# Kernel optimization log

Hardware: AMD Instinct MI355X
Metric: run time of the kernel (lower is better)

Reference implementation:

```python
import jax, jax.numpy as jnp
import numpy as np

NUM_USERS = 100000
NUM_ITEMS = 50000
EMBED_DIM = 64
N_LAYERS = 3
NNZ = 4800000
BATCH = 16384
N_NODES = NUM_USERS + NUM_ITEMS


def setup_inputs() -> dict:
    key = jax.random.key(0)
    k1, k2, k3, k4, k5, k6, k7 = jax.random.split(key, 7)
    users = jax.random.randint(k1, (BATCH,), 0, NUM_USERS, dtype=jnp.int64 if jax.config.jax_enable_x64 else jnp.int32)
    items = jax.random.randint(k2, (BATCH,), 0, NUM_ITEMS, dtype=jnp.int64 if jax.config.jax_enable_x64 else jnp.int32)
    adj_rows = jax.random.randint(k3, (NNZ,), 0, N_NODES, dtype=jnp.int32)
    adj_cols = jax.random.randint(k4, (NNZ,), 0, N_NODES, dtype=jnp.int32)
    adj_vals = jax.random.uniform(k5, (NNZ,), dtype=jnp.float32)
    user_emb = jax.random.normal(k6, (NUM_USERS, EMBED_DIM), dtype=jnp.float32)
    item_emb = jax.random.normal(k7, (NUM_ITEMS, EMBED_DIM), dtype=jnp.float32)
    return {"users": users, "items": items, "adj_rows": adj_rows,
            "adj_cols": adj_cols, "adj_vals": adj_vals,
            "user_emb": user_emb, "item_emb": item_emb}


def _spmm(rows, cols, vals, x):
    # y = A @ x for COO sparse A: gather source rows, scale, scatter-add to dest
    return jax.ops.segment_sum(vals[:, None] * x[cols], rows, num_segments=N_NODES)


def reference(users, items, adj_rows, adj_cols, adj_vals, user_emb, item_emb):
    ego = jnp.concatenate([user_emb, item_emb], axis=0)  # [N_NODES, D]
    acc = ego
    cur = ego
    for _ in range(N_LAYERS):
        cur = _spmm(adj_rows, adj_cols, adj_vals, cur)
        acc = acc + cur
    mean_emb = acc / jnp.float32(N_LAYERS + 1)
    user_final = mean_emb[:NUM_USERS]
    item_final = mean_emb[NUM_USERS:]
    u = user_final[users]  # [B, D]
    i = item_final[items]  # [B, D]
    return jnp.sum(u * i, axis=-1)  # [B]
```

## Files before the change

kernel.cpp:

```cpp
#include <hip/hip_runtime.h>
#include <hip/hip_bf16.h>

#define NUM_USERS 100000
#define NUM_ITEMS 50000
#define EMBED_DIM 64
#define N_NODES   150000
#define ROW_SHIFT 10
#define ROWS_PER_BUCKET 1024
#define B_BUCKETS ((N_NODES + ROWS_PER_BUCKET - 1) / ROWS_PER_BUCKET)
#define BIN_CHUNK 2048
#define COL_MASK 0x3FFFF
#define NSTRIPE 5
#define STRIPE_SHIFT 15

typedef unsigned short ushort_t;
typedef unsigned int uint_t;

__device__ __forceinline__ float bf16_to_f32(ushort_t u) {
    return __uint_as_float(((unsigned)u) << 16);
}
__device__ __forceinline__ ushort_t f32_to_bf16(float f) {
    return __builtin_bit_cast(ushort_t, __float2bfloat16(f));
}
__device__ __forceinline__ float bflo(uint_t r) {
    return __uint_as_float(r << 16);
}
__device__ __forceinline__ float bfhi(uint_t r) {
    return __uint_as_float(r & 0xffff0000u);
}

__global__ void k_bucket_hist(const int* __restrict__ rows, int* __restrict__ bhist, int nnz) {
    __shared__ int lh[256];
    int t = threadIdx.x;
    lh[t] = 0;
    __syncthreads();
    int base = blockIdx.x * (256 * 32);
#pragma unroll
    for (int k = 0; k < 32; k++) {
        int idx = base + k * 256 + t;
        if (idx < nnz) atomicAdd(&lh[rows[idx] >> ROW_SHIFT], 1);
    }
    __syncthreads();
    if (t < B_BUCKETS && lh[t] > 0) atomicAdd(&bhist[t], lh[t]);
}

__global__ void k_bucket_scan(const int* __restrict__ bhist, int* __restrict__ bucket_off,
                              int* __restrict__ bucket_cursor, int* __restrict__ offs, int nnz) {
    __shared__ int lds[256];
    int t = threadIdx.x;
    int v = (t < B_BUCKETS) ? bhist[t] : 0;
    lds[t] = v;
    __syncthreads();
    for (int d = 1; d < 256; d <<= 1) {
        int y = (t >= d) ? lds[t - d] : 0;
        __syncthreads();
        lds[t] += y;
        __syncthreads();
    }
    int excl = lds[t] - v;
    if (t < B_BUCKETS) {
        bucket_off[t] = excl;
        bucket_cursor[t] = excl;
    }
    if (t == 0) {
        bucket_off[B_BUCKETS] = nnz;
        offs[N_NODES] = nnz;
    }
}

__global__ void __launch_bounds__(256) k_bin(const int* __restrict__ rows,
                                             const int* __restrict__ cols,
                                             const float* __restrict__ vals,
                                             int* __restrict__ bucket_cursor,
                                             int2* __restrict__ staging, int nnz) {
    __shared__ int  ccnt[256];
    __shared__ int  cpos[256];
    __shared__ int  gdst[256];
    __shared__ int2 entries[BIN_CHUNK];
    __shared__ unsigned char ebuck[BIN_CHUNK];

    int t = threadIdx.x;
    int base = blockIdx.x * BIN_CHUNK;
    ccnt[t] = 0;
    __syncthreads();

    int myrow[BIN_CHUNK / 256];
#pragma unroll
    for (int k = 0; k < BIN_CHUNK / 256; k++) {
        int idx = base + k * 256 + t;
        int r = (idx < nnz) ? rows[idx] : -1;
        myrow[k] = r;
        if (r >= 0) atomicAdd(&ccnt[r >> ROW_SHIFT], 1);
    }
    __syncthreads();

    int c = ccnt[t];
    cpos[t] = c;
    __syncthreads();
    for (int d = 1; d < 256; d <<= 1) {
        int y = (t >= d) ? cpos[t - d] : 0;
        __syncthreads();
        cpos[t] += y;
        __syncthreads();
    }
    int total = cpos[255];
    int excl = cpos[t] - c;
    __syncthreads();
    cpos[t] = excl;
    __syncthreads();

#pragma unroll
    for (int k = 0; k < BIN_CHUNK / 256; k++) {
        int r = myrow[k];
        if (r >= 0) {
            int idx = base + k * 256 + t;
            int b = r >> ROW_SHIFT;
            int lrow = r & (ROWS_PER_BUCKET - 1);
            int slot = atomicAdd(&cpos[b], 1);
            entries[slot] = make_int2(cols[idx] | (lrow << 18), __float_as_int(vals[idx]));
            ebuck[slot] = (unsigned char)b;
        }
    }
    __syncthreads();

    if (t < B_BUCKETS && ccnt[t] > 0) {
        int g = atomicAdd(&bucket_cursor[t], ccnt[t]);
        gdst[t] = g - (cpos[t] - ccnt[t]);
    }
    __syncthreads();

    for (int i = t; i < total; i += 256) {
        staging[gdst[ebuck[i]] + i] = entries[i];
    }
}

__global__ void __launch_bounds__(1024) k_scatter2(const int2* __restrict__ staging,
                                                   const int* __restrict__ bucket_off,
                                                   int* __restrict__ offs,
                                                   int2* __restrict__ cv) {
    __shared__ int rc[ROWS_PER_BUCKET * NSTRIPE];
    __shared__ int sh[ROWS_PER_BUCKET];
    int b = blockIdx.x;
    int t = threadIdx.x;
    int beg = bucket_off[b], end = bucket_off[b + 1];
    int row0 = b << ROW_SHIFT;

#pragma unroll
    for (int s = 0; s < NSTRIPE; s++) rc[t * NSTRIPE + s] = 0;
    __syncthreads();
    for (int i = beg + t; i < end; i += 1024) {
        int ex = staging[i].x;
        int lrow = ex >> 18;
        int stripe = (ex & COL_MASK) >> STRIPE_SHIFT;
        atomicAdd(&rc[lrow * NSTRIPE + stripe], 1);
    }
    __syncthreads();

    int tot = 0;
#pragma unroll
    for (int s = 0; s < NSTRIPE; s++) tot += rc[t * NSTRIPE + s];
    sh[t] = tot;
    __syncthreads();
    for (int d = 1; d < 1024; d <<= 1) {
        int y = (t >= d) ? sh[t - d] : 0;
        __syncthreads();
        sh[t] += y;
        __syncthreads();
    }
    int excl_row = sh[t] - tot;
    int row = row0 + t;
    if (row < N_NODES) offs[row] = beg + excl_row;
    int basec = excl_row;
#pragma unroll
    for (int s = 0; s < NSTRIPE; s++) {
        int cnt = rc[t * NSTRIPE + s];
        rc[t * NSTRIPE + s] = basec;
        basec += cnt;
    }
    __syncthreads();

    for (int i = beg + t; i < end; i += 1024) {
        int2 e = staging[i];
        int lrow = e.x >> 18;
        int col = e.x & COL_MASK;
        int stripe = col >> STRIPE_SHIFT;
        int pos = beg + atomicAdd(&rc[lrow * NSTRIPE + stripe], 1);
        cv[pos] = make_int2(col, e.y);
    }
}

__global__ void k_convert(const float* __restrict__ ue, const float* __restrict__ ie,
                          ushort_t* __restrict__ xb) {
    int i = blockIdx.x * blockDim.x + threadIdx.x;
    const int n4 = (N_NODES * EMBED_DIM) / 4;
    if (i >= n4) return;
    const int usplit = (NUM_USERS * EMBED_DIM) / 4;
    float4 f = (i < usplit) ? ((const float4*)ue)[i] : ((const float4*)ie)[i - usplit];
    ushort4 o;
    o.x = f32_to_bf16(f.x);
    o.y = f32_to_bf16(f.y);
    o.z = f32_to_bf16(f.z);
    o.w = f32_to_bf16(f.w);
    ((ushort4*)xb)[i] = o;
}

__device__ __forceinline__ float2 spmm_row(int beg, int end, int hl, bool hi_half,
                                           const int2* __restrict__ cv,
                                           const ushort_t* __restrict__ xb) {
    const uint_t* __restrict__ xw = (const uint_t*)xb;
    float ax = 0.f, ay = 0.f;
    int e = beg;
    int npair = (end - beg) >> 1;
    int ng = npair >> 3;

    if (ng > 0) {
        uint_t r0[8], r1[8];
        float ve0[8], vo0[8], ve1[8], vo1[8];
#pragma unroll
        for (int j = 0; j < 8; j++) {
            int2 c0 = cv[e + 2 * j];
            int2 c1 = cv[e + 2 * j + 1];
            int ce = __builtin_amdgcn_readfirstlane(c0.x);
            int co = __builtin_amdgcn_readfirstlane(c1.x);
            ve0[j] = __int_as_float(__builtin_amdgcn_readfirstlane(c0.y));
            vo0[j] = __int_as_float(__builtin_amdgcn_readfirstlane(c1.y));
            int col = hi_half ? co : ce;
            r0[j] = xw[(size_t)col * 32 + hl];
        }
        e += 16;
#pragma unroll 1
        for (int g = 1; g < ng; g++) {
#pragma unroll
            for (int j = 0; j < 8; j++) {
                int2 c0 = cv[e + 2 * j];
                int2 c1 = cv[e + 2 * j + 1];
                int ce = __builtin_amdgcn_readfirstlane(c0.x);
                int co = __builtin_amdgcn_readfirstlane(c1.x);
                ve1[j] = __int_as_float(__builtin_amdgcn_readfirstlane(c0.y));
                vo1[j] = __int_as_float(__builtin_amdgcn_readfirstlane(c1.y));
                int col = hi_half ? co : ce;
                r1[j] = xw[(size_t)col * 32 + hl];
            }
            e += 16;
#pragma unroll
            for (int j = 0; j < 8; j++) {
                float v = hi_half ? vo0[j] : ve0[j];
                ax += v * bflo(r0[j]);
                ay += v * bfhi(r0[j]);
            }
#pragma unroll
            for (int j = 0; j < 8; j++) {
                r0[j] = r1[j]; ve0[j] = ve1[j]; vo0[j] = vo1[j];
            }
        }
#pragma unroll
        for (int j = 0; j < 8; j++) {
            float v = hi_half ? vo0[j] : ve0[j];
            ax += v * bflo(r0[j]);
            ay += v * bfhi(r0[j]);
        }
    }
#pragma unroll 1
    for (; e + 2 <= end; e += 2) {
        int2 c0 = cv[e];
        int2 c1 = cv[e + 1];
        int ce = __builtin_amdgcn_readfirstlane(c0.x);
        int co = __builtin_amdgcn_readfirstlane(c1.x);
        float ve = __int_as_float(__builtin_amdgcn_readfirstlane(c0.y));
        float vo = __int_as_float(__builtin_amdgcn_readfirstlane(c1.y));
        int col = hi_half ? co : ce;
        uint_t r = xw[(size_t)col * 32 + hl];
        float v = hi_half ? vo : ve;
        ax += v * bflo(r);
        ay += v * bfhi(r);
    }
    if (e < end) {
        int2 c = cv[e];
        int ce = __builtin_amdgcn_readfirstlane(c.x);
        float ve = __int_as_float(__builtin_amdgcn_readfirstlane(c.y));
        uint_t r = xw[(size_t)ce * 32 + hl];
        float v = hi_half ? 0.f : ve;
        ax += v * bflo(r);
        ay += v * bfhi(r);
    }
    ax += __shfl_xor(ax, 32, 64);
    ay += __shfl_xor(ay, 32, 64);
    return make_float2(ax, ay);
}

__global__ void k_spmm(const int* __restrict__ offs, const int2* __restrict__ cv,
                       const ushort_t* __restrict__ xb, ushort_t* __restrict__ out) {
    int row = (blockIdx.x * blockDim.x + threadIdx.x) >> 6;
    int lane = threadIdx.x & 63;
    if (row >= N_NODES) return;
    int hl = lane & 31;
    bool hi_half = lane >= 32;
    row = __builtin_amdgcn_readfirstlane(row);
    int beg = __builtin_amdgcn_readfirstlane(offs[row]);
    int end = __builtin_amdgcn_readfirstlane(offs[row + 1]);
    float2 a = spmm_row(beg, end, hl, hi_half, cv, xb);
    if (!hi_half) {
        uint_t packed = ((uint_t)f32_to_bf16(a.y) << 16) | (uint_t)f32_to_bf16(a.x);
        ((uint_t*)out)[(size_t)row * 32 + hl] = packed;
    }
}

__global__ void k_spmm_batch(const int* __restrict__ offs, const int2* __restrict__ cv,
                             const ushort_t* __restrict__ xb,
                             const int* __restrict__ users, const int* __restrict__ items,
                             float* __restrict__ u_acc, float* __restrict__ i_acc,
                             int batch) {
    int w = (blockIdx.x * blockDim.x + threadIdx.x) >> 6;
    int lane = threadIdx.x & 63;
    if (w >= 2 * batch) return;
    int hl = lane & 31;
    bool hi_half = lane >= 32;
    int b, row;
    float* dst;
    if (w < batch) { b = w;         row = users[b];             dst = u_acc; }
    else           { b = w - batch; row = NUM_USERS + items[b]; dst = i_acc; }
    row = __builtin_amdgcn_readfirstlane(row);
    int beg = __builtin_amdgcn_readfirstlane(offs[row]);
    int end = __builtin_amdgcn_readfirstlane(offs[row + 1]);
    float2 a = spmm_row(beg, end, hl, hi_half, cv, xb);
    if (!hi_half) {
        float2* d = (float2*)(dst + (size_t)b * EMBED_DIM) + hl;
        float2 cur = *d;
        cur.x += a.x;
        cur.y += a.y;
        *d = cur;
    }
}

__global__ void k_gather_f32(const int* __restrict__ users, const int* __restrict__ items,
                             const float* __restrict__ ue, const float* __restrict__ ie,
                             float* __restrict__ u_acc, float* __restrict__ i_acc, int batch) {
    int w = (blockIdx.x * blockDim.x + threadIdx.x) >> 6;
    int lane = threadIdx.x & 63;
    if (w >= batch) return;
    int nu = users[w];
    int ni = items[w];
    size_t o = (size_t)w * EMBED_DIM + lane;
    u_acc[o] = ue[(size_t)nu * EMBED_DIM + lane];
    i_acc[o] = ie[(size_t)ni * EMBED_DIM + lane];
}

__global__ void k_gather_bf16(const int* __restrict__ users, const int* __restrict__ items,
                              const ushort_t* __restrict__ xb,
                              float* __restrict__ u_acc, float* __restrict__ i_acc, int batch) {
    int w = (blockIdx.x * blockDim.x + threadIdx.x) >> 6;
    int lane = threadIdx.x & 63;
    if (w >= batch) return;
    int nu = users[w];
    int ni = NUM_USERS + items[w];
    size_t o = (size_t)w * EMBED_DIM + lane;
    u_acc[o] += bf16_to_f32(xb[(size_t)nu * EMBED_DIM + lane]);
    i_acc[o] += bf16_to_f32(xb[(size_t)ni * EMBED_DIM + lane]);
}

__global__ void k_dot(const float* __restrict__ u_acc, const float* __restrict__ i_acc,
                      float* __restrict__ out, int batch) {
    int w = (blockIdx.x * blockDim.x + threadIdx.x) >> 6;
    int lane = threadIdx.x & 63;
    if (w >= batch) return;
    size_t o = (size_t)w * EMBED_DIM + lane;
    float p = u_acc[o] * i_acc[o];
#pragma unroll
    for (int d = 32; d > 0; d >>= 1) p += __shfl_down(p, d, 64);
    if (lane == 0) out[w] = p * (1.0f / 16.0f);
}


extern "C" void kernel_launch(void* const* d_in, const int* in_sizes, int n_in,
                              void* d_out, int out_size, void* d_ws, size_t ws_size,
                              hipStream_t stream) {
    const int*   users    = (const int*)  d_in[0];
    const int*   items    = (const int*)  d_in[1];
    const int*   adj_rows = (const int*)  d_in[2];
    const int*   adj_cols = (const int*)  d_in[3];
    const float* adj_vals = (const float*)d_in[4];
    const float* user_emb = (const float*)d_in[5];
    const float* item_emb = (const float*)d_in[6];
    float* out = (float*)d_out;

    const int batch = in_sizes[0];
    const int nnz   = in_sizes[2];

    char* p = (char*)d_ws;
    auto alloc = [&](size_t bytes) -> char* {
        char* r = p;
        p += (bytes + 255) & ~(size_t)255;
        return r;
    };
    const size_t xb_bytes = (size_t)N_NODES * EMBED_DIM * 2;
    int*      offs          = (int*)  alloc(((size_t)N_NODES + 1) * 4);
    int*      bhist         = (int*)  alloc(256 * 4);
    int*      bucket_off    = (int*)  alloc(256 * 4);
    int*      bucket_cursor = (int*)  alloc(256 * 4);
    int2*     cv            = (int2*) alloc((size_t)nnz * 8);
    size_t    region_bytes  = (size_t)nnz * 8;
    if (region_bytes < 2 * xb_bytes) region_bytes = 2 * xb_bytes;
    char*     region        = alloc(region_bytes);
    int2*     staging       = (int2*)region;
    ushort_t* xbA           = (ushort_t*)region;
    ushort_t* xbB           = (ushort_t*)(region + xb_bytes);
    ushort_t* xb_ego        = (ushort_t*)alloc(xb_bytes);
    float*    u_acc         = (float*)alloc((size_t)batch * EMBED_DIM * 4);
    float*    i_acc         = (float*)alloc((size_t)batch * EMBED_DIM * 4);

    const int g_bhist  = (nnz + 256 * 32 - 1) / (256 * 32);
    const int g_bin    = (nnz + BIN_CHUNK - 1) / BIN_CHUNK;
    const int g_conv   = ((N_NODES * EMBED_DIM / 4) + 255) / 256;
    const int g_nodes  = (N_NODES + 3) / 4;
    const int g_batch  = (batch + 3) / 4;
    const int g_batch2 = (2 * batch + 3) / 4;

    hipMemsetAsync(bhist, 0, 256 * 4, stream);
    k_bucket_hist<<<g_bhist, 256, 0, stream>>>(adj_rows, bhist, nnz);
    k_bucket_scan<<<1, 256, 0, stream>>>(bhist, bucket_off, bucket_cursor, offs, nnz);
    k_bin<<<g_bin, 256, 0, stream>>>(adj_rows, adj_cols, adj_vals, bucket_cursor, staging, nnz);
    k_scatter2<<<B_BUCKETS, 1024, 0, stream>>>(staging, bucket_off, offs, cv);

    k_convert<<<g_conv, 256, 0, stream>>>(user_emb, item_emb, xb_ego);

    k_gather_f32<<<g_batch, 256, 0, stream>>>(users, items, user_emb, item_emb,
                                              u_acc, i_acc, batch);

    k_spmm<<<g_nodes, 256, 0, stream>>>(offs, cv, xb_ego, xbA);
    k_gather_bf16<<<g_batch, 256, 0, stream>>>(users, items, xbA, u_acc, i_acc, batch);

    k_spmm<<<g_nodes, 256, 0, stream>>>(offs, cv, xbA, xbB);
    k_gather_bf16<<<g_batch, 256, 0, stream>>>(users, items, xbB, u_acc, i_acc, batch);

    k_spmm_batch<<<g_batch2, 256, 0, stream>>>(offs, cv, xbB, users, items,
                                               u_acc, i_acc, batch);

    k_dot<<<g_batch, 256, 0, stream>>>(u_acc, i_acc, out, batch);
}
```

Baseline: 512.8 us.

## Halve bucket size, drop column striping in CSR build, double-buffer SpMM loads

The COO-to-CSR bucketing now uses 512-row buckets (293 buckets) with 512-thread blocks, and removes the per-row column-stripe sub-sort in the scatter kernel, so each bucket does a plain per-row count, scan and scatter. The SpMM inner loop drops the register copy between groups by alternating two load buffers, and it accumulates into a float2 vector type so the compiler can emit packed FMA. The CSR build should get cheaper in exchange for losing column locality within each row, which may hurt gather cache reuse in the SpMM passes.

```diff
diff --git a/kernel.cpp b/kernel.cpp
--- a/kernel.cpp
+++ b/kernel.cpp
@@ -5,16 +5,16 @@
 #define NUM_ITEMS 50000
 #define EMBED_DIM 64
 #define N_NODES   150000
-#define ROW_SHIFT 10
-#define ROWS_PER_BUCKET 1024
+#define ROW_SHIFT 9
+#define ROWS_PER_BUCKET 512
 #define B_BUCKETS ((N_NODES + ROWS_PER_BUCKET - 1) / ROWS_PER_BUCKET)
+#define NBP 512
 #define BIN_CHUNK 2048
 #define COL_MASK 0x3FFFF
-#define NSTRIPE 5
-#define STRIPE_SHIFT 15
 
 typedef unsigned short ushort_t;
 typedef unsigned int uint_t;
+typedef float v2f __attribute__((ext_vector_type(2)));
 
 __device__ __forceinline__ float bf16_to_f32(ushort_t u) {
     return __uint_as_float(((unsigned)u) << 16);
@@ -29,29 +29,32 @@
     return __uint_as_float(r & 0xffff0000u);
 }
 
-__global__ void k_bucket_hist(const int* __restrict__ rows, int* __restrict__ bhist, int nnz) {
-    __shared__ int lh[256];
+__global__ void __launch_bounds__(512) k_bucket_hist(const int* __restrict__ rows,
+                                                     int* __restrict__ bhist, int nnz) {
+    __shared__ int lh[NBP];
     int t = threadIdx.x;
     lh[t] = 0;
     __syncthreads();
-    int base = blockIdx.x * (256 * 32);
+    int base = blockIdx.x * (512 * 32);
 #pragma unroll
     for (int k = 0; k < 32; k++) {
-        int idx = base + k * 256 + t;
+        int idx = base + k * 512 + t;
         if (idx < nnz) atomicAdd(&lh[rows[idx] >> ROW_SHIFT], 1);
     }
     __syncthreads();
     if (t < B_BUCKETS && lh[t] > 0) atomicAdd(&bhist[t], lh[t]);
 }
 
-__global__ void k_bucket_scan(const int* __restrict__ bhist, int* __restrict__ bucket_off,
-                              int* __restrict__ bucket_cursor, int* __restrict__ offs, int nnz) {
-    __shared__ int lds[256];
+__global__ void __launch_bounds__(512) k_bucket_scan(const int* __restrict__ bhist,
+                                                     int* __restrict__ bucket_off,
+                                                     int* __restrict__ bucket_cursor,
+                                                     int* __restrict__ offs, int nnz) {
+    __shared__ int lds[NBP];
     int t = threadIdx.x;
     int v = (t < B_BUCKETS) ? bhist[t] : 0;
     lds[t] = v;
     __syncthreads();
-    for (int d = 1; d < 256; d <<= 1) {
+    for (int d = 1; d < NBP; d <<= 1) {
         int y = (t >= d) ? lds[t - d] : 0;
         __syncthreads();
         lds[t] += y;
@@ -68,26 +71,26 @@
     }
 }
 
-__global__ void __launch_bounds__(256) k_bin(const int* __restrict__ rows,
+__global__ void __launch_bounds__(512) k_bin(const int* __restrict__ rows,
                                              const int* __restrict__ cols,
                                              const float* __restrict__ vals,
                                              int* __restrict__ bucket_cursor,
                                              int2* __restrict__ staging, int nnz) {
-    __shared__ int  ccnt[256];
-    __shared__ int  cpos[256];
-    __shared__ int  gdst[256];
+    __shared__ int  ccnt[NBP];
+    __shared__ int  cpos[NBP];
+    __shared__ int  gdst[NBP];
     __shared__ int2 entries[BIN_CHUNK];
-    __shared__ unsigned char ebuck[BIN_CHUNK];
+    __shared__ ushort_t ebuck[BIN_CHUNK];
 
     int t = threadIdx.x;
     int base = blockIdx.x * BIN_CHUNK;
     ccnt[t] = 0;
     __syncthreads();
 
-    int myrow[BIN_CHUNK / 256];
-#pragma unroll
-    for (int k = 0; k < BIN_CHUNK / 256; k++) {
-        int idx = base + k * 256 + t;
+    int myrow[BIN_CHUNK / 512];
+#pragma unroll
+    for (int k = 0; k < BIN_CHUNK / 512; k++) {
+        int idx = base + k * 512 + t;
         int r = (idx < nnz) ? rows[idx] : -1;
         myrow[k] = r;
         if (r >= 0) atomicAdd(&ccnt[r >> ROW_SHIFT], 1);
@@ -97,28 +100,28 @@
     int c = ccnt[t];
     cpos[t] = c;
     __syncthreads();
-    for (int d = 1; d < 256; d <<= 1) {
+    for (int d = 1; d < NBP; d <<= 1) {
         int y = (t >= d) ? cpos[t - d] : 0;
         __syncthreads();
         cpos[t] += y;
         __syncthreads();
     }
-    int total = cpos[255];
+    int total = cpos[NBP - 1];
     int excl = cpos[t] - c;
     __syncthreads();
     cpos[t] = excl;
     __syncthreads();
 
 #pragma unroll
-    for (int k = 0; k < BIN_CHUNK / 256; k++) {
+    for (int k = 0; k < BIN_CHUNK / 512; k++) {
         int r = myrow[k];
         if (r >= 0) {
-            int idx = base + k * 256 + t;
+            int idx = base + k * 512 + t;
             int b = r >> ROW_SHIFT;
             int lrow = r & (ROWS_PER_BUCKET - 1);
             int slot = atomicAdd(&cpos[b], 1);
             entries[slot] = make_int2(cols[idx] | (lrow << 18), __float_as_int(vals[idx]));
-            ebuck[slot] = (unsigned char)b;
+            ebuck[slot] = (ushort_t)b;
         }
     }
     __syncthreads();
@@ -129,63 +132,45 @@
     }
     __syncthreads();
 
-    for (int i = t; i < total; i += 256) {
+    for (int i = t; i < total; i += 512) {
         staging[gdst[ebuck[i]] + i] = entries[i];
     }
 }
 
-__global__ void __launch_bounds__(1024) k_scatter2(const int2* __restrict__ staging,
-                                                   const int* __restrict__ bucket_off,
-                                                   int* __restrict__ offs,
-                                                   int2* __restrict__ cv) {
-    __shared__ int rc[ROWS_PER_BUCKET * NSTRIPE];
-    __shared__ int sh[ROWS_PER_BUCKET];
+__global__ void __launch_bounds__(512) k_scatter2(const int2* __restrict__ staging,
+                                                  const int* __restrict__ bucket_off,
+                                                  int* __restrict__ offs,
+                                                  int2* __restrict__ cv) {
+    __shared__ int rc[ROWS_PER_BUCKET];
     int b = blockIdx.x;
     int t = threadIdx.x;
     int beg = bucket_off[b], end = bucket_off[b + 1];
     int row0 = b << ROW_SHIFT;
 
-#pragma unroll
-    for (int s = 0; s < NSTRIPE; s++) rc[t * NSTRIPE + s] = 0;
-    __syncthreads();
-    for (int i = beg + t; i < end; i += 1024) {
-        int ex = staging[i].x;
-        int lrow = ex >> 18;
-        int stripe = (ex & COL_MASK) >> STRIPE_SHIFT;
-        atomicAdd(&rc[lrow * NSTRIPE + stripe], 1);
-    }
-    __syncthreads();
-
-    int tot = 0;
-#pragma unroll
-    for (int s = 0; s < NSTRIPE; s++) tot += rc[t * NSTRIPE + s];
-    sh[t] = tot;
-    __syncthreads();
-    for (int d = 1; d < 1024; d <<= 1) {
-        int y = (t >= d) ? sh[t - d] : 0;
-        __syncthreads();
-        sh[t] += y;
-        __syncthreads();
-    }
-    int excl_row = sh[t] - tot;
+    rc[t] = 0;
+    __syncthreads();
+    for (int i = beg + t; i < end; i += 512)
+        atomicAdd(&rc[staging[i].x >> 18], 1);
+    __syncthreads();
+
+    int c = rc[t];
+    for (int d = 1; d < ROWS_PER_BUCKET; d <<= 1) {
+        int y = (t >= d) ? rc[t - d] : 0;
+        __syncthreads();
+        rc[t] += y;
+        __syncthreads();
+    }
+    int excl = rc[t] - c;
     int row = row0 + t;
-    if (row < N_NODES) offs[row] = beg + excl_row;
-    int basec = excl_row;
-#pragma unroll
-    for (int s = 0; s < NSTRIPE; s++) {
-        int cnt = rc[t * NSTRIPE + s];
-        rc[t * NSTRIPE + s] = basec;
-        basec += cnt;
-    }
-    __syncthreads();
-
-    for (int i = beg + t; i < end; i += 1024) {
+    if (row < N_NODES) offs[row] = beg + excl;
+    __syncthreads();
+    rc[t] = excl;
+    __syncthreads();
+
+    for (int i = beg + t; i < end; i += 512) {
         int2 e = staging[i];
-        int lrow = e.x >> 18;
-        int col = e.x & COL_MASK;
-        int stripe = col >> STRIPE_SHIFT;
-        int pos = beg + atomicAdd(&rc[lrow * NSTRIPE + stripe], 1);
-        cv[pos] = make_int2(col, e.y);
+        int pos = beg + atomicAdd(&rc[e.x >> 18], 1);
+        cv[pos] = make_int2(e.x & COL_MASK, e.y);
     }
 }
 
@@ -204,11 +189,43 @@
     ((ushort4*)xb)[i] = o;
 }
 
+__device__ __forceinline__ void ld_group8(int e, int hl, bool hi_half,
+                                          const int2* __restrict__ cv,
+                                          const uint_t* __restrict__ xw,
+                                          uint_t r[8], float ve[8], float vo[8]) {
+#pragma unroll
+    for (int j = 0; j < 8; j++) {
+        int2 c0 = cv[e + 2 * j];
+        int2 c1 = cv[e + 2 * j + 1];
+        int ce = __builtin_amdgcn_readfirstlane(c0.x);
+        int co = __builtin_amdgcn_readfirstlane(c1.x);
+        ve[j] = __int_as_float(__builtin_amdgcn_readfirstlane(c0.y));
+        vo[j] = __int_as_float(__builtin_amdgcn_readfirstlane(c1.y));
+        int col = hi_half ? co : ce;
+        r[j] = xw[(size_t)col * 32 + hl];
+    }
+}
+
+__device__ __forceinline__ void fma_group8(v2f& acc, bool hi_half,
+                                           const uint_t r[8],
+                                           const float ve[8], const float vo[8]) {
+#pragma unroll
+    for (int j = 0; j < 8; j++) {
+        float v = hi_half ? vo[j] : ve[j];
+        v2f x;
+        x.x = bflo(r[j]);
+        x.y = bfhi(r[j]);
+        acc += x * v;
+    }
+}
+
 __device__ __forceinline__ float2 spmm_row(int beg, int end, int hl, bool hi_half,
                                            const int2* __restrict__ cv,
                                            const ushort_t* __restrict__ xb) {
     const uint_t* __restrict__ xw = (const uint_t*)xb;
-    float ax = 0.f, ay = 0.f;
+    v2f acc;
+    acc.x = 0.f;
+    acc.y = 0.f;
     int e = beg;
     int npair = (end - beg) >> 1;
     int ng = npair >> 3;
@@ -216,48 +233,25 @@
     if (ng > 0) {
         uint_t r0[8], r1[8];
         float ve0[8], vo0[8], ve1[8], vo1[8];
-#pragma unroll
-        for (int j = 0; j < 8; j++) {
-            int2 c0 = cv[e + 2 * j];
-            int2 c1 = cv[e + 2 * j + 1];
-            int ce = __builtin_amdgcn_readfirstlane(c0.x);
-            int co = __builtin_amdgcn_readfirstlane(c1.x);
-            ve0[j] = __int_as_float(__builtin_amdgcn_readfirstlane(c0.y));
-            vo0[j] = __int_as_float(__builtin_amdgcn_readfirstlane(c1.y));
-            int col = hi_half ? co : ce;
-            r0[j] = xw[(size_t)col * 32 + hl];
+        ld_group8(e, hl, hi_half, cv, xw, r0, ve0, vo0);
+        e += 16;
+        int g = 1;
+#pragma unroll 1
+        for (; g + 1 < ng; g += 2) {
+            ld_group8(e, hl, hi_half, cv, xw, r1, ve1, vo1);
+            e += 16;
+            fma_group8(acc, hi_half, r0, ve0, vo0);
+            ld_group8(e, hl, hi_half, cv, xw, r0, ve0, vo0);
+            e += 16;
+            fma_group8(acc, hi_half, r1, ve1, vo1);
         }
-        e += 16;
-#pragma unroll 1
-        for (int g = 1; g < ng; g++) {
-#pragma unroll
-            for (int j = 0; j < 8; j++) {
-                int2 c0 = cv[e + 2 * j];
-                int2 c1 = cv[e + 2 * j + 1];
-                int ce = __builtin_amdgcn_readfirstlane(c0.x);
-                int co = __builtin_amdgcn_readfirstlane(c1.x);
-                ve1[j] = __int_as_float(__builtin_amdgcn_readfirstlane(c0.y));
-                vo1[j] = __int_as_float(__builtin_amdgcn_readfirstlane(c1.y));
-                int col = hi_half ? co : ce;
-                r1[j] = xw[(size_t)col * 32 + hl];
-            }
+        if (g < ng) {
+            ld_group8(e, hl, hi_half, cv, xw, r1, ve1, vo1);
             e += 16;
-#pragma unroll
-            for (int j = 0; j < 8; j++) {
-                float v = hi_half ? vo0[j] : ve0[j];
-                ax += v * bflo(r0[j]);
-                ay += v * bfhi(r0[j]);
-            }
-#pragma unroll
-            for (int j = 0; j < 8; j++) {
-                r0[j] = r1[j]; ve0[j] = ve1[j]; vo0[j] = vo1[j];
-            }
-        }
-#pragma unroll
-        for (int j = 0; j < 8; j++) {
-            float v = hi_half ? vo0[j] : ve0[j];
-            ax += v * bflo(r0[j]);
-            ay += v * bfhi(r0[j]);
+            fma_group8(acc, hi_half, r0, ve0, vo0);
+            fma_group8(acc, hi_half, r1, ve1, vo1);
+        } else {
+            fma_group8(acc, hi_half, r0, ve0, vo0);
         }
     }
 #pragma unroll 1
@@ -266,23 +260,24 @@
         int2 c1 = cv[e + 1];
         int ce = __builtin_amdgcn_readfirstlane(c0.x);
         int co = __builtin_amdgcn_readfirstlane(c1.x);
-        float ve = __int_as_float(__builtin_amdgcn_readfirstlane(c0.y));
-        float vo = __int_as_float(__builtin_amdgcn_readfirstlane(c1.y));
+        float vee = __int_as_float(__builtin_amdgcn_readfirstlane(c0.y));
+        float voo = __int_as_float(__builtin_amdgcn_readfirstlane(c1.y));
         int col = hi_half ? co : ce;
         uint_t r = xw[(size_t)col * 32 + hl];
-        float v = hi_half ? vo : ve;
-        ax += v * bflo(r);
-        ay += v * bfhi(r);
+        float v = hi_half ? voo : vee;
+        acc.x += v * bflo(r);
+        acc.y += v * bfhi(r);
     }
     if (e < end) {
         int2 c = cv[e];
         int ce = __builtin_amdgcn_readfirstlane(c.x);
-        float ve = __int_as_float(__builtin_amdgcn_readfirstlane(c.y));
+        float vee = __int_as_float(__builtin_amdgcn_readfirstlane(c.y));
         uint_t r = xw[(size_t)ce * 32 + hl];
-        float v = hi_half ? 0.f : ve;
-        ax += v * bflo(r);
-        ay += v * bfhi(r);
-    }
+        float v = hi_half ? 0.f : vee;
+        acc.x += v * bflo(r);
+        acc.y += v * bfhi(r);
+    }
+    float ax = acc.x, ay = acc.y;
     ax += __shfl_xor(ax, 32, 64);
     ay += __shfl_xor(ay, 32, 64);
     return make_float2(ax, ay);
@@ -394,9 +389,9 @@
     };
     const size_t xb_bytes = (size_t)N_NODES * EMBED_DIM * 2;
     int*      offs          = (int*)  alloc(((size_t)N_NODES + 1) * 4);
-    int*      bhist         = (int*)  alloc(256 * 4);
-    int*      bucket_off    = (int*)  alloc(256 * 4);
-    int*      bucket_cursor = (int*)  alloc(256 * 4);
+    int*      bhist         = (int*)  alloc(NBP * 4);
+    int*      bucket_off    = (int*)  alloc((NBP + 1) * 4);
+    int*      bucket_cursor = (int*)  alloc(NBP * 4);
     int2*     cv            = (int2*) alloc((size_t)nnz * 8);
     size_t    region_bytes  = (size_t)nnz * 8;
     if (region_bytes < 2 * xb_bytes) region_bytes = 2 * xb_bytes;
@@ -408,18 +403,18 @@
     float*    u_acc         = (float*)alloc((size_t)batch * EMBED_DIM * 4);
     float*    i_acc         = (float*)alloc((size_t)batch * EMBED_DIM * 4);
 
-    const int g_bhist  = (nnz + 256 * 32 - 1) / (256 * 32);
+    const int g_bhist  = (nnz + 512 * 32 - 1) / (512 * 32);
     const int g_bin    = (nnz + BIN_CHUNK - 1) / BIN_CHUNK;
     const int g_conv   = ((N_NODES * EMBED_DIM / 4) + 255) / 256;
     const int g_nodes  = (N_NODES + 3) / 4;
     const int g_batch  = (batch + 3) / 4;
     const int g_batch2 = (2 * batch + 3) / 4;
 
-    hipMemsetAsync(bhist, 0, 256 * 4, stream);
-    k_bucket_hist<<<g_bhist, 256, 0, stream>>>(adj_rows, bhist, nnz);
-    k_bucket_scan<<<1, 256, 0, stream>>>(bhist, bucket_off, bucket_cursor, offs, nnz);
-    k_bin<<<g_bin, 256, 0, stream>>>(adj_rows, adj_cols, adj_vals, bucket_cursor, staging, nnz);
-    k_scatter2<<<B_BUCKETS, 1024, 0, stream>>>(staging, bucket_off, offs, cv);
+    hipMemsetAsync(bhist, 0, NBP * 4, stream);
+    k_bucket_hist<<<g_bhist, 512, 0, stream>>>(adj_rows, bhist, nnz);
+    k_bucket_scan<<<1, 512, 0, stream>>>(bhist, bucket_off, bucket_cursor, offs, nnz);
+    k_bin<<<g_bin, 512, 0, stream>>>(adj_rows, adj_cols, adj_vals, bucket_cursor, staging, nnz);
+    k_scatter2<<<B_BUCKETS, 512, 0, stream>>>(staging, bucket_off, offs, cv);
 
     k_convert<<<g_conv, 256, 0, stream>>>(user_emb, item_emb, xb_ego);
 
```

New measurement: 509.0 us. About the same (-0.7%).
